# Optimization experiments

Measured on AMD Instinct MI355X. Metric: run time of the kernel, lower is better.

## Reference

```python
import jax, jax.numpy as jnp
import numpy as np

B, T, P, W = 32, 4096, 512, 1024  # batch, time, param_size, width


def setup_inputs() -> dict:
    key = jax.random.key(0)
    ks = jax.random.split(key, 9)
    lim = 1.0 / np.sqrt(W).astype(np.float32)
    lim = float(lim)
    u = lambda k, shape, l: jax.random.uniform(k, shape, minval=-l, maxval=l, dtype=jnp.float32)
    a = jax.random.normal(ks[0], (B, T, P), dtype=jnp.float32)
    h0 = u(ks[1], (W,), lim)
    weight_ih = u(ks[2], (3 * W, P), lim)
    weight_hh = u(ks[3], (3 * W, W), lim)
    bias = u(ks[4], (3 * W,), lim)
    bias_n = u(ks[5], (W,), lim)
    lim_o = float(1.0 / np.sqrt(W))
    w_out = u(ks[6], (P, W), lim_o)
    b_out = u(ks[7], (P,), lim_o)
    return {"a": a, "h0": h0, "weight_ih": weight_ih, "weight_hh": weight_hh,
            "bias": bias, "bias_n": bias_n, "w_out": w_out, "b_out": b_out}


def _encode(a, h0, weight_ih, weight_hh, bias, bias_n, w_out, b_out):
    # Precompute input gates for all steps (big GEMM, hoisted out of the scan).
    # ig: [B, T, 3W]
    ig = jnp.einsum('btp,gp->btg', a, weight_ih) + bias

    def step(h, ig_t):
        # h: [B, W], ig_t: [B, 3W]
        hg = h @ weight_hh.T                       # [B, 3W]
        ig_r, ig_z, ig_n = jnp.split(ig_t, 3, axis=-1)
        hg_r, hg_z, hg_n = jnp.split(hg, 3, axis=-1)
        r = jax.nn.sigmoid(ig_r + hg_r)
        z = jax.nn.sigmoid(ig_z + hg_z)
        n = jnp.tanh(ig_n + r * (hg_n + bias_n))
        h_new = n + z * (h - n)                    # equinox GRUCell update
        return h_new, h_new

    h_init = jnp.broadcast_to(h0, (a.shape[0], h0.shape[0]))
    # scan over time (reverse), batched inside: xs [T, B, 3W]
    _, hs = jax.lax.scan(step, h_init, jnp.swapaxes(ig, 0, 1), reverse=True)
    hs = jnp.swapaxes(hs, 0, 1)                    # [B, T, W]
    return hs @ w_out.T + b_out                    # [B, T, P]


def reference(a, h0, weight_ih, weight_hh, bias, bias_n, w_out, b_out):
    return _encode(a, h0, weight_ih, weight_hh, bias, bias_n, w_out, b_out)
```

## Files before the change

### kernel.cpp

```cpp
#include <hip/hip_runtime.h>
#include <cstddef>

#define TT 4096
#define PP 512
#define WW 1024

using u32 = unsigned;
using u64 = unsigned long long;
using u16 = unsigned short;

typedef short short8 __attribute__((ext_vector_type(8)));
typedef float f32x4 __attribute__((ext_vector_type(4)));

__device__ __forceinline__ u32 bfround(float f) {
    u32 u = __float_as_uint(f);
    return (u + 0x7fffu + ((u >> 16) & 1u)) >> 16;
}
__device__ __forceinline__ float bf2f(u32 q) { return __uint_as_float(q << 16); }
__device__ __forceinline__ float bflo(u32 q) { return __uint_as_float(q << 16); }
__device__ __forceinline__ float bfhi(u32 q) { return __uint_as_float(q & 0xffff0000u); }

#define LDA64(p)    __hip_atomic_load((p),  __ATOMIC_RELAXED, __HIP_MEMORY_SCOPE_AGENT)
#define STA64(p, v) __hip_atomic_store((p), (v), __ATOMIC_RELAXED, __HIP_MEMORY_SCOPE_AGENT)
#define LDA32(p)    __hip_atomic_load((p),  __ATOMIC_RELAXED, __HIP_MEMORY_SCOPE_AGENT)
#define STA32(p, v) __hip_atomic_store((p), (v), __ATOMIC_RELAXED, __HIP_MEMORY_SCOPE_AGENT)
#define STA16(p, v) __hip_atomic_store((p), (v), __ATOMIC_RELAXED, __HIP_MEMORY_SCOPE_AGENT)

__global__ __launch_bounds__(256) void a2bf(const float* __restrict__ a, u16* __restrict__ abf) {
    const size_t i = ((size_t)blockIdx.x * 256 + threadIdx.x) * 8;
    float4 lo = *(const float4*)&a[i];
    float4 hi = *(const float4*)&a[i + 4];
    uint4 w;
    w.x = bfround(lo.x) | (bfround(lo.y) << 16);
    w.y = bfround(lo.z) | (bfround(lo.w) << 16);
    w.z = bfround(hi.x) | (bfround(hi.y) << 16);
    w.w = bfround(hi.z) | (bfround(hi.w) << 16);
    *(uint4*)&abf[i] = w;
}

__global__ __launch_bounds__(768, 1) void ig_prepass8(
    const u16* __restrict__ abf, const float* __restrict__ Wih,
    const float* __restrict__ bias, char* __restrict__ igbase)
{
    const int gp  = blockIdx.x;
    const int t0  = blockIdx.y * 64;
    const int tid = threadIdx.x;
    const int lane = tid & 63;
    const int wid  = tid >> 6;

    short8 af[2][16];
    float  bi[2][4];
    int    gWGv[2], slotv[2];
    #pragma unroll
    for (int rt2 = 0; rt2 < 2; ++rt2) {
        const int rowb = gp * 384 + rt2 * 192 + wid * 16;
        const float* wr = &Wih[(size_t)(rowb + (lane & 15)) * PP + (lane >> 4) * 8];
        #pragma unroll
        for (int s = 0; s < 16; ++s) {
            float t8[8];
            *(float4*)&t8[0] = *(const float4*)&wr[s * 32];
            *(float4*)&t8[4] = *(const float4*)&wr[s * 32 + 4];
            #pragma unroll
            for (int j = 0; j < 8; ++j) af[rt2][s][j] = (short)bfround(t8[j]);
        }
        const int grow0 = rowb + (lane >> 4) * 4;
        #pragma unroll
        for (int r = 0; r < 4; ++r) bi[rt2][r] = bias[grow0 + r];
        const int gate = grow0 >> 10, w = grow0 & 1023;
        gWGv[rt2] = w >> 4;
        slotv[rt2] = gate * 16 + (w & 15);
    }
    const int bcol = lane & 15;

    for (int ct = 0; ct < 128; ++ct) {
        const int t = t0 + (ct >> 1);
        const int b = (ct & 1) * 16 + bcol;
        const u16* ap = &abf[((size_t)b * TT + t) * PP + (lane >> 4) * 8];
        f32x4 d0 = {0.f, 0.f, 0.f, 0.f}, d1 = {0.f, 0.f, 0.f, 0.f};
        #pragma unroll 4
        for (int s = 0; s < 16; ++s) {
            short8 bf = *(const short8*)&ap[s * 32];
            d0 = __builtin_amdgcn_mfma_f32_16x16x32_bf16(af[0][s], bf, d0, 0, 0, 0);
            d1 = __builtin_amdgcn_mfma_f32_16x16x32_bf16(af[1][s], bf, d1, 0, 0, 0);
        }
        u32 l0 = bfround(d0[0] + bi[0][0]) | (bfround(d0[1] + bi[0][1]) << 16);
        u32 h0_ = bfround(d0[2] + bi[0][2]) | (bfround(d0[3] + bi[0][3]) << 16);
        u32 l1 = bfround(d1[0] + bi[1][0]) | (bfround(d1[1] + bi[1][1]) << 16);
        u32 h1_ = bfround(d1[2] + bi[1][2]) | (bfround(d1[3] + bi[1][3]) << 16);
        *(u64*)(igbase + (((size_t)t * 64 + gWGv[0]) * 1536 + (size_t)b * 48 + slotv[0]) * 2) = (u64)l0 | ((u64)h0_ << 32);
        *(u64*)(igbase + (((size_t)t * 64 + gWGv[1]) * 1536 + (size_t)b * 48 + slotv[1]) * 2) = (u64)l1 | ((u64)h1_ << 32);
    }
}

__global__ __launch_bounds__(768, 1) void ig_prepass16(
    const float* __restrict__ a, const float* __restrict__ Wih,
    const float* __restrict__ bias, char* __restrict__ igbase)
{
    const int gp   = blockIdx.x;
    const int t0   = blockIdx.y * 64;
    const int tid  = threadIdx.x;
    const int lane = tid & 63;
    const int wid  = tid >> 6;
    const int growb = gp * 192 + wid * 16;

    short8 afrag[16];
    float  biasv[4];
    {
        const float* wr = &Wih[(size_t)(growb + (lane & 15)) * PP + (lane >> 4) * 8];
        #pragma unroll
        for (int s = 0; s < 16; ++s) {
            float t8[8];
            *(float4*)&t8[0] = *(const float4*)&wr[s * 32];
            *(float4*)&t8[4] = *(const float4*)&wr[s * 32 + 4];
            #pragma unroll
            for (int j = 0; j < 8; ++j) afrag[s][j] = (short)bfround(t8[j]);
        }
        #pragma unroll
        for (int r = 0; r < 4; ++r) biasv[r] = bias[growb + (lane >> 4) * 4 + r];
    }
    const int grow0 = growb + (lane >> 4) * 4;
    const int gate  = grow0 >> 10;
    const int w     = grow0 & 1023;
    const int gWG   = w >> 4;
    const int slot  = gate * 16 + (w & 15);
    const int bcol  = lane & 15;

    for (int ct = 0; ct < 128; ++ct) {
        const int t = t0 + (ct >> 1);
        const int b = (ct & 1) * 16 + bcol;
        const float* ap = &a[((size_t)b * TT + t) * PP + (lane >> 4) * 8];
        f32x4 d = {0.f, 0.f, 0.f, 0.f};
        #pragma unroll 4
        for (int s = 0; s < 16; ++s) {
            float4 lo = *(const float4*)&ap[s * 32];
            float4 hi = *(const float4*)&ap[s * 32 + 4];
            short8 bfv;
            bfv[0] = (short)((__float_as_uint(lo.x) + 0x8000u) >> 16);
            bfv[1] = (short)((__float_as_uint(lo.y) + 0x8000u) >> 16);
            bfv[2] = (short)((__float_as_uint(lo.z) + 0x8000u) >> 16);
            bfv[3] = (short)((__float_as_uint(lo.w) + 0x8000u) >> 16);
            bfv[4] = (short)((__float_as_uint(hi.x) + 0x8000u) >> 16);
            bfv[5] = (short)((__float_as_uint(hi.y) + 0x8000u) >> 16);
            bfv[6] = (short)((__float_as_uint(hi.z) + 0x8000u) >> 16);
            bfv[7] = (short)((__float_as_uint(hi.w) + 0x8000u) >> 16);
            d = __builtin_amdgcn_mfma_f32_16x16x32_bf16(afrag[s], bfv, d, 0, 0, 0);
        }
        u32 lo32 = bfround(d[0] + biasv[0]) | (bfround(d[1] + biasv[1]) << 16);
        u32 hi32 = bfround(d[2] + biasv[2]) | (bfround(d[3] + biasv[3]) << 16);
        *(u64*)(igbase + (((size_t)t * 64 + gWG) * 1536 + (size_t)b * 48 + slot) * 2) =
            (u64)lo32 | ((u64)hi32 << 32);
    }
}

__global__ __launch_bounds__(768, 1) void gru_scan4(
    const float* __restrict__ h0v, const float* __restrict__ Whh,
    const float* __restrict__ bias_n, const float* __restrict__ Wout,
    const float* __restrict__ bout, const char* __restrict__ igbase,
    float* __restrict__ out, u64* __restrict__ bufA, u64* __restrict__ bufB,
    u32* __restrict__ flags)
{
    __shared__ float sPreH[4][48][2][17];
    __shared__ float sOutP[4][16][18];
    __shared__ __align__(8) u64 sIgRaw[384];

    const int g    = blockIdx.x;
    const int tid  = threadIdx.x;
    const int lane = tid & 63;
    const int wid  = tid >> 6;
    const int p0   = (g >> 1) * 16;
    const int pb0  = (g & 1) * 16;

    short8 frag[24];
    if (wid < 8) {
        const int kq = wid & 3;
        #pragma unroll
        for (int gate = 0; gate < 3; ++gate)
            #pragma unroll
            for (int s = 0; s < 8; ++s) {
                const float* wr = &Whh[(size_t)(gate * WW + g * 16 + (lane & 15)) * WW
                                       + (kq * 8 + s) * 32 + (lane >> 4) * 8];
                float t8[8];
                *(float4*)&t8[0] = *(const float4*)&wr[0];
                *(float4*)&t8[4] = *(const float4*)&wr[4];
                short8 v;
                #pragma unroll
                for (int j = 0; j < 8; ++j) v[j] = (short)bfround(t8[j]);
                frag[gate * 8 + s] = v;
            }
    } else {
        const int kq3 = wid - 8;
        #pragma unroll
        for (int s = 0; s < 8; ++s) {
            const float* wr = &Wout[(size_t)(p0 + (lane & 15)) * WW
                                    + (kq3 * 8 + s) * 32 + (lane >> 4) * 8];
            float t8[8];
            *(float4*)&t8[0] = *(const float4*)&wr[0];
            *(float4*)&t8[4] = *(const float4*)&wr[4];
            short8 v;
            #pragma unroll
            for (int j = 0; j < 8; ++j) v[j] = (short)bfround(t8[j]);
            frag[s] = v;
        }
    }

    float h_own = 0.f, bnv = 0.f;
    int gwl = 0, gb = 0; u32 hidx16 = 0;
    if (tid >= 256) {
        const int idx = tid - 256;
        gwl = idx & 15; gb = idx >> 4;
        h_own = h0v[g * 16 + gwl];
        bnv   = bias_n[g * 16 + gwl];
        const int w_abs = g * 16 + gwl;
        const int ip = (w_abs >> 3) * 64 + 2 * gb + ((w_abs >> 2) & 1);
        hidx16 = 4 * ip + (w_abs & 3);
        STA16(&((u16*)bufA)[hidx16], (u16)bfround(h_own));
    }
    const float boutp = (tid < 256) ? bout[p0 + (tid & 15)] : 0.f;

    const int fo_hh = (lane >> 4) * 32 + ((wid >> 2) & 1) * 16 + (lane & 15);
    const int fo_p3 = (lane >> 4) * 32 + pb0 + (lane & 15);

    u64* hcur = bufA;
    u64* hnxt = bufB;
    u32 kk = 1;

    for (int t = TT - 1; t >= 0; --t) {
        if (wid >= 4) asm volatile("s_waitcnt vmcnt(0)" ::: "memory");
        __syncthreads();
        if (tid == 0) STA32(&flags[g * 16], kk);

        u64 igr = 0;
        if (tid < 384) igr = *(const u64*)(igbase + ((size_t)t * 64 + g) * 3072 + tid * 8);

        for (;;) {
            u32 v = LDA32(&flags[lane * 16]);
            if (__all((int)(v - kk) >= 0)) break;
            __builtin_amdgcn_s_sleep(1);
        }
        asm volatile("" ::: "memory");

        if (wid < 8) {
            const int kq = wid & 3;
            f32x4 c0 = {0.f,0.f,0.f,0.f}, c1 = {0.f,0.f,0.f,0.f}, c2 = {0.f,0.f,0.f,0.f};
            #pragma unroll
            for (int s = 0; s < 8; ++s) {
                const int ss = kq * 8 + s;
                const u64 q0 = LDA64(&hcur[2 * (ss * 128 + fo_hh)]);
                const u64 q1 = LDA64(&hcur[2 * (ss * 128 + fo_hh) + 1]);
                union { u64 q[2]; short8 v; } uu; uu.q[0] = q0; uu.q[1] = q1;
                c0 = __builtin_amdgcn_mfma_f32_16x16x32_bf16(frag[s],      uu.v, c0, 0, 0, 0);
                c1 = __builtin_amdgcn_mfma_f32_16x16x32_bf16(frag[8 + s],  uu.v, c1, 0, 0, 0);
                c2 = __builtin_amdgcn_mfma_f32_16x16x32_bf16(frag[16 + s], uu.v, c2, 0, 0, 0);
            }
            const int bt = wid >> 2, r0 = (lane >> 4) * 4, col = lane & 15;
            #pragma unroll
            for (int r = 0; r < 4; ++r) {
                sPreH[kq][r0 + r][bt][col]      = c0[r];
                sPreH[kq][16 + r0 + r][bt][col] = c1[r];
                sPreH[kq][32 + r0 + r][bt][col] = c2[r];
            }
        } else {
            const int kq3 = wid - 8;
            f32x4 d = {0.f, 0.f, 0.f, 0.f};
            #pragma unroll
            for (int s = 0; s < 8; ++s) {
                const int ss = kq3 * 8 + s;
                const u64 q0 = LDA64(&hcur[2 * (ss * 128 + fo_p3)]);
                const u64 q1 = LDA64(&hcur[2 * (ss * 128 + fo_p3) + 1]);
                union { u64 q[2]; short8 v; } uu; uu.q[0] = q0; uu.q[1] = q1;
                d = __builtin_amdgcn_mfma_f32_16x16x32_bf16(frag[s], uu.v, d, 0, 0, 0);
            }
            const int r0 = (lane >> 4) * 4, col = lane & 15;
            #pragma unroll
            for (int r = 0; r < 4; ++r) sOutP[kq3][r0 + r][col] = d[r];
        }
        if (tid < 384) sIgRaw[tid] = igr;
        __syncthreads();

        if (tid >= 256) {
            const u16* sIgU = (const u16*)sIgRaw;
            const float ig_r = bf2f(sIgU[gb * 48 + gwl]);
            const float ig_z = bf2f(sIgU[gb * 48 + 16 + gwl]);
            const float ig_n = bf2f(sIgU[gb * 48 + 32 + gwl]);
            const int bh = gb >> 4, bc = gb & 15;
            const float hg_r = sPreH[0][gwl][bh][bc] + sPreH[1][gwl][bh][bc]
                             + sPreH[2][gwl][bh][bc] + sPreH[3][gwl][bh][bc];
            const float hg_z = sPreH[0][16 + gwl][bh][bc] + sPreH[1][16 + gwl][bh][bc]
                             + sPreH[2][16 + gwl][bh][bc] + sPreH[3][16 + gwl][bh][bc];
            const float hg_n = sPreH[0][32 + gwl][bh][bc] + sPreH[1][32 + gwl][bh][bc]
                             + sPreH[2][32 + gwl][bh][bc] + sPreH[3][32 + gwl][bh][bc];
            const float rr = __builtin_amdgcn_rcpf(1.f + __expf(-(ig_r + hg_r)));
            const float zz = __builtin_amdgcn_rcpf(1.f + __expf(-(ig_z + hg_z)));
            const float xn = ig_n + rr * (hg_n + bnv);
            const float nn = 2.f * __builtin_amdgcn_rcpf(1.f + __expf(-2.f * xn)) - 1.f;
            h_own = nn + zz * (h_own - nn);
            STA16(&((u16*)hnxt)[hidx16], (u16)bfround(h_own));
        } else if (t < TT - 1) {
            const int p = tid & 15, b = tid >> 4;
            const float s_ = boutp + sOutP[0][p][b] + sOutP[1][p][b]
                                   + sOutP[2][p][b] + sOutP[3][p][b];
            out[((size_t)(pb0 + b) * TT + (t + 1)) * PP + p0 + p] = s_;
        }

        u64* tmp = hcur; hcur = hnxt; hnxt = tmp;
        ++kk;
    }

    if (wid >= 4) asm volatile("s_waitcnt vmcnt(0)" ::: "memory");
    __syncthreads();
    if (tid == 0) STA32(&flags[g * 16], kk);
    if (wid >= 8) {
        for (;;) {
            u32 v = LDA32(&flags[lane * 16]);
            if (__all((int)(v - kk) >= 0)) break;
            __builtin_amdgcn_s_sleep(1);
        }
        asm volatile("" ::: "memory");
        const int kq3 = wid - 8;
        f32x4 d = {0.f, 0.f, 0.f, 0.f};
        #pragma unroll
        for (int s = 0; s < 8; ++s) {
            const int ss = kq3 * 8 + s;
            const u64 q0 = LDA64(&hcur[2 * (ss * 128 + fo_p3)]);
            const u64 q1 = LDA64(&hcur[2 * (ss * 128 + fo_p3) + 1]);
            union { u64 q[2]; short8 v; } uu; uu.q[0] = q0; uu.q[1] = q1;
            d = __builtin_amdgcn_mfma_f32_16x16x32_bf16(frag[s], uu.v, d, 0, 0, 0);
        }
        const int r0 = (lane >> 4) * 4, col = lane & 15;
        #pragma unroll
        for (int r = 0; r < 4; ++r) sOutP[kq3][r0 + r][col] = d[r];
    }
    __syncthreads();
    if (tid < 256) {
        const int p = tid & 15, b = tid >> 4;
        const float s_ = boutp + sOutP[0][p][b] + sOutP[1][p][b]
                               + sOutP[2][p][b] + sOutP[3][p][b];
        out[((size_t)(pb0 + b) * TT) * PP + p0 + p] = s_;
    }
}

__device__ __forceinline__ void grid_barrier32(u32* leaf, u32* root, u32 rtarget, int g) {
    asm volatile("s_waitcnt vmcnt(0)" ::: "memory");
    __syncthreads();
    if (threadIdx.x == 0) {
        u32 old = __hip_atomic_fetch_add(&leaf[(g & 7) * 16], 1u,
                                         __ATOMIC_RELAXED, __HIP_MEMORY_SCOPE_AGENT);
        if ((old & 31u) == 31u)
            __hip_atomic_fetch_add(root, 1u, __ATOMIC_RELAXED, __HIP_MEMORY_SCOPE_AGENT);
        while (__hip_atomic_load(root, __ATOMIC_RELAXED, __HIP_MEMORY_SCOPE_AGENT) < rtarget)
            __builtin_amdgcn_s_sleep(2);
    }
    __syncthreads();
}

__global__ __launch_bounds__(768, 1) void gru_scan_fb(
    const float* __restrict__ a, const float* __restrict__ h0,
    const float* __restrict__ Wih, const float* __restrict__ Whh,
    const float* __restrict__ bias, const float* __restrict__ bias_n,
    const float* __restrict__ Wout, const float* __restrict__ bout,
    float* __restrict__ out, u64* __restrict__ hbufA, u64* __restrict__ hbufB,
    u32* __restrict__ leaf, u32* __restrict__ root)
{
    __shared__ float sWhh[12][WW];
    __shared__ __align__(16) u64 sh[8192];
    __shared__ float sPreH[2][12][32];
    __shared__ float sIg[2][2][12][32];
    __shared__ float sOutPart[12][64];

    const int g   = blockIdx.x;
    const int tid = threadIdx.x;
// ... 142 lines not shown
        r5 = LDH(5); r6 = LDH(6); r7 = LDH(7); r8 = LDH(8); r9 = LDH(9);
        if (tid < 512) r10 = LDH(10);
        #undef LDH
        sh[tid] = r0;          sh[tid + 768] = r1;   sh[tid + 1536] = r2;
        sh[tid + 2304] = r3;   sh[tid + 3072] = r4;  sh[tid + 3840] = r5;
        sh[tid + 4608] = r6;   sh[tid + 5376] = r7;  sh[tid + 6144] = r8;
        sh[tid + 6912] = r9;
        if (tid < 512) sh[tid + 7680] = r10;
        __syncthreads();
        p3partials();
        __syncthreads();
        if (tid < 64) {
            float s_ = boutv;
            #pragma unroll
            for (int cc = 0; cc < 12; ++cc) s_ += sOutPart[cc][o];
            out[((size_t)p3b * TT) * PP + p3p] = s_;
        }
    }
}

extern "C" void kernel_launch(void* const* d_in, const int* in_sizes, int n_in,
                              void* d_out, int out_size, void* d_ws, size_t ws_size,
                              hipStream_t stream) {
    const float* a      = (const float*)d_in[0];
    const float* h0     = (const float*)d_in[1];
    const float* Wih    = (const float*)d_in[2];
    const float* Whh    = (const float*)d_in[3];
    const float* bias   = (const float*)d_in[4];
    const float* bias_n = (const float*)d_in[5];
    const float* Wout   = (const float*)d_in[6];
    const float* bout   = (const float*)d_in[7];
    float* out = (float*)d_out;

    const size_t IG_BYTES  = (size_t)TT * 64 * 3072;
    const size_t ABF_BYTES = (size_t)32 * TT * PP * 2;
    const size_t NEED_FULL = IG_BYTES + ABF_BYTES + 2 * 65536 + 4096;
    const size_t NEED_MID  = IG_BYTES + 2 * 65536 + 4096;

    if (ws_size >= NEED_FULL) {
        char* igbase = (char*)d_ws;
        u16*  abf    = (u16*)((char*)d_ws + IG_BYTES);
        u64*  bufA   = (u64*)((char*)d_ws + IG_BYTES + ABF_BYTES);
        u64*  bufB   = bufA + 8192;
        u32*  flags  = (u32*)((char*)d_ws + IG_BYTES + ABF_BYTES + 2 * 65536);
        hipMemsetAsync(flags, 0, 4096, stream);
        hipLaunchKernelGGL(a2bf, dim3(32768), dim3(256), 0, stream, a, abf);
        hipLaunchKernelGGL(ig_prepass8, dim3(8, 64), dim3(768), 0, stream,
                           abf, Wih, bias, igbase);
        void* args[] = {(void*)&h0, (void*)&Whh, (void*)&bias_n, (void*)&Wout,
                        (void*)&bout, (void*)&igbase, (void*)&out,
                        (void*)&bufA, (void*)&bufB, (void*)&flags};
        hipLaunchCooperativeKernel((void*)gru_scan4, dim3(64), dim3(768),
                                   args, 0, stream);
    } else if (ws_size >= NEED_MID) {
        char* igbase = (char*)d_ws;
        u64*  bufA   = (u64*)((char*)d_ws + IG_BYTES);
        u64*  bufB   = bufA + 8192;
        u32*  flags  = (u32*)((char*)d_ws + IG_BYTES + 2 * 65536);
        hipMemsetAsync(flags, 0, 4096, stream);
        hipLaunchKernelGGL(ig_prepass16, dim3(16, 64), dim3(768), 0, stream,
                           a, Wih, bias, igbase);
        void* args[] = {(void*)&h0, (void*)&Whh, (void*)&bias_n, (void*)&Wout,
                        (void*)&bout, (void*)&igbase, (void*)&out,
                        (void*)&bufA, (void*)&bufB, (void*)&flags};
        hipLaunchCooperativeKernel((void*)gru_scan4, dim3(64), dim3(768),
                                   args, 0, stream);
    } else {
        u64* hA   = (u64*)d_ws;
        u64* hB   = hA + 8192;
        u32* leaf = (u32*)((char*)d_ws + 2 * 65536);
        u32* root = leaf + 8 * 16;
        hipMemsetAsync(leaf, 0, 1024, stream);
        void* args[] = {(void*)&a, (void*)&h0, (void*)&Wih, (void*)&Whh,
                        (void*)&bias, (void*)&bias_n, (void*)&Wout, (void*)&bout,
                        (void*)&out, (void*)&hA, (void*)&hB, (void*)&leaf, (void*)&root};
        hipLaunchCooperativeKernel((void*)gru_scan_fb, dim3(256), dim3(768),
                                   args, 0, stream);
    }
}
```

Before: 20.30 ms.

## Fuse input-gate GEMM producer blocks with GRU scan in one cooperative kernel

Replaces the separate a-to-bf16 conversion, input-gate prepass and scan kernels with a single cooperative kernel of 256 blocks. Blocks 0-63 run the recurrence while the other blocks compute the input-gate GEMM per 64-step chunk in reverse time order and signal readiness through counters. The old global flag barrier is replaced by tagged h values that consumers poll until the step tag matches, and the output projection is folded into the same MFMA loop. This overlaps the large prepass with the serial scan and removes launches and the bf16 staging buffer, at the cost of spin-wait polling, more register pressure, and producers that can fall behind the scan.

```diff
diff --git a/kernel.cpp b/kernel.cpp
--- a/kernel.cpp
+++ b/kernel.cpp
@@ -24,155 +24,43 @@
 #define STA64(p, v) __hip_atomic_store((p), (v), __ATOMIC_RELAXED, __HIP_MEMORY_SCOPE_AGENT)
 #define LDA32(p)    __hip_atomic_load((p),  __ATOMIC_RELAXED, __HIP_MEMORY_SCOPE_AGENT)
 #define STA32(p, v) __hip_atomic_store((p), (v), __ATOMIC_RELAXED, __HIP_MEMORY_SCOPE_AGENT)
-#define STA16(p, v) __hip_atomic_store((p), (v), __ATOMIC_RELAXED, __HIP_MEMORY_SCOPE_AGENT)
-
-__global__ __launch_bounds__(256) void a2bf(const float* __restrict__ a, u16* __restrict__ abf) {
-    const size_t i = ((size_t)blockIdx.x * 256 + threadIdx.x) * 8;
-    float4 lo = *(const float4*)&a[i];
-    float4 hi = *(const float4*)&a[i + 4];
-    uint4 w;
-    w.x = bfround(lo.x) | (bfround(lo.y) << 16);
-    w.y = bfround(lo.z) | (bfround(lo.w) << 16);
-    w.z = bfround(hi.x) | (bfround(hi.y) << 16);
-    w.w = bfround(hi.z) | (bfround(hi.w) << 16);
-    *(uint4*)&abf[i] = w;
-}
-
-__global__ __launch_bounds__(768, 1) void ig_prepass8(
-    const u16* __restrict__ abf, const float* __restrict__ Wih,
-    const float* __restrict__ bias, char* __restrict__ igbase)
-{
-    const int gp  = blockIdx.x;
-    const int t0  = blockIdx.y * 64;
-    const int tid = threadIdx.x;
-    const int lane = tid & 63;
-    const int wid  = tid >> 6;
-
-    short8 af[2][16];
-    float  bi[2][4];
-    int    gWGv[2], slotv[2];
-    #pragma unroll
-    for (int rt2 = 0; rt2 < 2; ++rt2) {
-        const int rowb = gp * 384 + rt2 * 192 + wid * 16;
-        const float* wr = &Wih[(size_t)(rowb + (lane & 15)) * PP + (lane >> 4) * 8];
-        #pragma unroll
-        for (int s = 0; s < 16; ++s) {
-            float t8[8];
-            *(float4*)&t8[0] = *(const float4*)&wr[s * 32];
-            *(float4*)&t8[4] = *(const float4*)&wr[s * 32 + 4];
-            #pragma unroll
-            for (int j = 0; j < 8; ++j) af[rt2][s][j] = (short)bfround(t8[j]);
-        }
-        const int grow0 = rowb + (lane >> 4) * 4;
-        #pragma unroll
-        for (int r = 0; r < 4; ++r) bi[rt2][r] = bias[grow0 + r];
-        const int gate = grow0 >> 10, w = grow0 & 1023;
-        gWGv[rt2] = w >> 4;
-        slotv[rt2] = gate * 16 + (w & 15);
-    }
-    const int bcol = lane & 15;
-
-    for (int ct = 0; ct < 128; ++ct) {
-        const int t = t0 + (ct >> 1);
-        const int b = (ct & 1) * 16 + bcol;
-        const u16* ap = &abf[((size_t)b * TT + t) * PP + (lane >> 4) * 8];
-        f32x4 d0 = {0.f, 0.f, 0.f, 0.f}, d1 = {0.f, 0.f, 0.f, 0.f};
-        #pragma unroll 4
-        for (int s = 0; s < 16; ++s) {
-            short8 bf = *(const short8*)&ap[s * 32];
-            d0 = __builtin_amdgcn_mfma_f32_16x16x32_bf16(af[0][s], bf, d0, 0, 0, 0);
-            d1 = __builtin_amdgcn_mfma_f32_16x16x32_bf16(af[1][s], bf, d1, 0, 0, 0);
-        }
-        u32 l0 = bfround(d0[0] + bi[0][0]) | (bfround(d0[1] + bi[0][1]) << 16);
-        u32 h0_ = bfround(d0[2] + bi[0][2]) | (bfround(d0[3] + bi[0][3]) << 16);
-        u32 l1 = bfround(d1[0] + bi[1][0]) | (bfround(d1[1] + bi[1][1]) << 16);
-        u32 h1_ = bfround(d1[2] + bi[1][2]) | (bfround(d1[3] + bi[1][3]) << 16);
-        *(u64*)(igbase + (((size_t)t * 64 + gWGv[0]) * 1536 + (size_t)b * 48 + slotv[0]) * 2) = (u64)l0 | ((u64)h0_ << 32);
-        *(u64*)(igbase + (((size_t)t * 64 + gWGv[1]) * 1536 + (size_t)b * 48 + slotv[1]) * 2) = (u64)l1 | ((u64)h1_ << 32);
-    }
-}
-
-__global__ __launch_bounds__(768, 1) void ig_prepass16(
-    const float* __restrict__ a, const float* __restrict__ Wih,
-    const float* __restrict__ bias, char* __restrict__ igbase)
-{
-    const int gp   = blockIdx.x;
-    const int t0   = blockIdx.y * 64;
-    const int tid  = threadIdx.x;
-    const int lane = tid & 63;
-    const int wid  = tid >> 6;
-    const int growb = gp * 192 + wid * 16;
-
-    short8 afrag[16];
-    float  biasv[4];
-    {
-        const float* wr = &Wih[(size_t)(growb + (lane & 15)) * PP + (lane >> 4) * 8];
-        #pragma unroll
-        for (int s = 0; s < 16; ++s) {
-            float t8[8];
-            *(float4*)&t8[0] = *(const float4*)&wr[s * 32];
-            *(float4*)&t8[4] = *(const float4*)&wr[s * 32 + 4];
-            #pragma unroll
-            for (int j = 0; j < 8; ++j) afrag[s][j] = (short)bfround(t8[j]);
-        }
-        #pragma unroll
-        for (int r = 0; r < 4; ++r) biasv[r] = bias[growb + (lane >> 4) * 4 + r];
-    }
-    const int grow0 = growb + (lane >> 4) * 4;
-    const int gate  = grow0 >> 10;
-    const int w     = grow0 & 1023;
-    const int gWG   = w >> 4;
-    const int slot  = gate * 16 + (w & 15);
-    const int bcol  = lane & 15;
-
-    for (int ct = 0; ct < 128; ++ct) {
-        const int t = t0 + (ct >> 1);
-        const int b = (ct & 1) * 16 + bcol;
-        const float* ap = &a[((size_t)b * TT + t) * PP + (lane >> 4) * 8];
-        f32x4 d = {0.f, 0.f, 0.f, 0.f};
-        #pragma unroll 4
-        for (int s = 0; s < 16; ++s) {
-            float4 lo = *(const float4*)&ap[s * 32];
-            float4 hi = *(const float4*)&ap[s * 32 + 4];
-            short8 bfv;
-            bfv[0] = (short)((__float_as_uint(lo.x) + 0x8000u) >> 16);
-            bfv[1] = (short)((__float_as_uint(lo.y) + 0x8000u) >> 16);
-            bfv[2] = (short)((__float_as_uint(lo.z) + 0x8000u) >> 16);
-            bfv[3] = (short)((__float_as_uint(lo.w) + 0x8000u) >> 16);
-            bfv[4] = (short)((__float_as_uint(hi.x) + 0x8000u) >> 16);
-            bfv[5] = (short)((__float_as_uint(hi.y) + 0x8000u) >> 16);
-            bfv[6] = (short)((__float_as_uint(hi.z) + 0x8000u) >> 16);
-            bfv[7] = (short)((__float_as_uint(hi.w) + 0x8000u) >> 16);
-            d = __builtin_amdgcn_mfma_f32_16x16x32_bf16(afrag[s], bfv, d, 0, 0, 0);
-        }
-        u32 lo32 = bfround(d[0] + biasv[0]) | (bfround(d[1] + biasv[1]) << 16);
-        u32 hi32 = bfround(d[2] + biasv[2]) | (bfround(d[3] + biasv[3]) << 16);
-        *(u64*)(igbase + (((size_t)t * 64 + gWG) * 1536 + (size_t)b * 48 + slot) * 2) =
-            (u64)lo32 | ((u64)hi32 << 32);
-    }
-}
-
-__global__ __launch_bounds__(768, 1) void gru_scan4(
-    const float* __restrict__ h0v, const float* __restrict__ Whh,
-    const float* __restrict__ bias_n, const float* __restrict__ Wout,
-    const float* __restrict__ bout, const char* __restrict__ igbase,
-    float* __restrict__ out, u64* __restrict__ bufA, u64* __restrict__ bufB,
-    u32* __restrict__ flags)
+
+#define TAGM 0x00001FFF00001FFFull
+
+__global__ __launch_bounds__(512, 2) void gru_fused(
+    const float* __restrict__ a,
+    const float* __restrict__ h0v,
+    const float* __restrict__ Wih,
+    const float* __restrict__ Whh,
+    const float* __restrict__ bias,
+    const float* __restrict__ bias_n,
+    const float* __restrict__ Wout,
+    const float* __restrict__ bout,
+    char* __restrict__ igbase,
+    float* __restrict__ out,
+    u64* __restrict__ bufA, u64* __restrict__ bufB,
+    u32* __restrict__ igready)
 {
     __shared__ float sPreH[4][48][2][17];
     __shared__ float sOutP[4][16][18];
     __shared__ __align__(8) u64 sIgRaw[384];
-
-    const int g    = blockIdx.x;
+    __shared__ __align__(16) u16 aLds[16][520];
+
+    const int bid  = blockIdx.x;
     const int tid  = threadIdx.x;
     const int lane = tid & 63;
     const int wid  = tid >> 6;
-    const int p0   = (g >> 1) * 16;
-    const int pb0  = (g & 1) * 16;
-
-    short8 frag[24];
-    if (wid < 8) {
-        const int kq = wid & 3;
+
+    if (bid < 64) {
+        const int g   = bid;
+        const int kq  = wid & 3;
+        const int bt  = wid >> 2;
+        const int p0  = (g >> 1) * 16;
+        const int pb0 = (g & 1) * 16;
+        const bool isP3 = (bt == (g & 1));
+        const int colb  = bt * 16 + (lane & 15);
+
+        short8 fragR[8], fragZ[8], fragN[8], fragP[8];
         #pragma unroll
         for (int gate = 0; gate < 3; ++gate)
             #pragma unroll
@@ -185,157 +73,268 @@
                 short8 v;
                 #pragma unroll
                 for (int j = 0; j < 8; ++j) v[j] = (short)bfround(t8[j]);
-                frag[gate * 8 + s] = v;
-            }
-    } else {
-        const int kq3 = wid - 8;
-        #pragma unroll
-        for (int s = 0; s < 8; ++s) {
-            const float* wr = &Wout[(size_t)(p0 + (lane & 15)) * WW
-                                    + (kq3 * 8 + s) * 32 + (lane >> 4) * 8];
-            float t8[8];
-            *(float4*)&t8[0] = *(const float4*)&wr[0];
-            *(float4*)&t8[4] = *(const float4*)&wr[4];
-            short8 v;
-            #pragma unroll
-            for (int j = 0; j < 8; ++j) v[j] = (short)bfround(t8[j]);
-            frag[s] = v;
-        }
-    }
-
-    float h_own = 0.f, bnv = 0.f;
-    int gwl = 0, gb = 0; u32 hidx16 = 0;
-    if (tid >= 256) {
-        const int idx = tid - 256;
-        gwl = idx & 15; gb = idx >> 4;
-        h_own = h0v[g * 16 + gwl];
-        bnv   = bias_n[g * 16 + gwl];
-        const int w_abs = g * 16 + gwl;
-        const int ip = (w_abs >> 3) * 64 + 2 * gb + ((w_abs >> 2) & 1);
-        hidx16 = 4 * ip + (w_abs & 3);
-        STA16(&((u16*)bufA)[hidx16], (u16)bfround(h_own));
-    }
-    const float boutp = (tid < 256) ? bout[p0 + (tid & 15)] : 0.f;
-
-    const int fo_hh = (lane >> 4) * 32 + ((wid >> 2) & 1) * 16 + (lane & 15);
-    const int fo_p3 = (lane >> 4) * 32 + pb0 + (lane & 15);
-
-    u64* hcur = bufA;
-    u64* hnxt = bufB;
-    u32 kk = 1;
-
-    for (int t = TT - 1; t >= 0; --t) {
-        if (wid >= 4) asm volatile("s_waitcnt vmcnt(0)" ::: "memory");
+                if (gate == 0) fragR[s] = v; else if (gate == 1) fragZ[s] = v; else fragN[s] = v;
+            }
+        if (isP3) {
+            #pragma unroll
+            for (int s = 0; s < 8; ++s) {
+                const float* wr = &Wout[(size_t)(p0 + (lane & 15)) * WW
+                                        + (kq * 8 + s) * 32 + (lane >> 4) * 8];
+                float t8[8];
+                *(float4*)&t8[0] = *(const float4*)&wr[0];
+                *(float4*)&t8[4] = *(const float4*)&wr[4];
+                short8 v;
+                #pragma unroll
+                for (int j = 0; j < 8; ++j) v[j] = (short)bfround(t8[j]);
+                fragP[s] = v;
+            }
+        }
+
+        const int gwl = tid & 15, gb = tid >> 4;
+        float h_own = h0v[g * 16 + gwl];
+        const float bnv = bias_n[g * 16 + gwl];
+        const int pubW = (g * 2 + (gwl >> 3)) * 256 + gb * 8 + (gwl & 7);
+        const float boutp = (tid < 256) ? bout[p0 + (tid & 15)] : 0.f;
+
+        STA32(&((u32*)bufA)[pubW], (bfround(h_own) << 16) | 4097u);
+
+        u64* cur = bufA;
+        u64* nxt = bufB;
+
+        for (int t = TT - 1; t >= 0; --t) {
+            if ((t & 63) == 63 && tid < 384) {
+                while (LDA32(&igready[(t >> 6) * 16]) < 8u)
+                    __builtin_amdgcn_s_sleep(8);
+            }
+            u64 igr = 0;
+            if (tid < 384) igr = *(const u64*)(igbase + ((size_t)t * 64 + g) * 3072 + tid * 8);
+
+            const u32 tg = (u32)(t + 2);
+            const u64 want2 = (u64)tg | ((u64)tg << 32);
+            f32x4 cR = {0.f,0.f,0.f,0.f}, cZ = {0.f,0.f,0.f,0.f};
+            f32x4 cN = {0.f,0.f,0.f,0.f}, cP = {0.f,0.f,0.f,0.f};
+            #pragma unroll
+            for (int grp = 0; grp < 2; ++grp) {
+                u64 q[16];
+                #pragma unroll
+                for (int s4 = 0; s4 < 4; ++s4) {
+                    const int ss = kq * 8 + grp * 4 + s4;
+                    const int ub = (ss * 4 + (lane >> 4)) * 128 + colb * 4;
+                    #pragma unroll
+                    for (int j = 0; j < 4; ++j) q[s4 * 4 + j] = LDA64(&cur[ub + j]);
+                }
+                bool ok;
+                do {
+                    ok = true;
+                    #pragma unroll
+                    for (int s4 = 0; s4 < 4; ++s4) {
+                        const int ss = kq * 8 + grp * 4 + s4;
+                        const int ub = (ss * 4 + (lane >> 4)) * 128 + colb * 4;
+                        #pragma unroll
+                        for (int j = 0; j < 4; ++j)
+                            if (((q[s4 * 4 + j] ^ want2) & TAGM) != 0ull) {
+                                q[s4 * 4 + j] = LDA64(&cur[ub + j]); ok = false;
+                            }
+                    }
+                } while (!__all(ok));
+                #pragma unroll
+                for (int s4 = 0; s4 < 4; ++s4) {
+                    const int s = grp * 4 + s4;
+                    const u64 a0 = q[s4*4+0], a1 = q[s4*4+1], a2 = q[s4*4+2], a3 = q[s4*4+3];
+                    short8 bv;
+                    bv[0] = (short)((u32)a0 >> 16); bv[1] = (short)(a0 >> 48);
+                    bv[2] = (short)((u32)a1 >> 16); bv[3] = (short)(a1 >> 48);
+                    bv[4] = (short)((u32)a2 >> 16); bv[5] = (short)(a2 >> 48);
+                    bv[6] = (short)((u32)a3 >> 16); bv[7] = (short)(a3 >> 48);
+                    cR = __builtin_amdgcn_mfma_f32_16x16x32_bf16(fragR[s], bv, cR, 0, 0, 0);
+                    cZ = __builtin_amdgcn_mfma_f32_16x16x32_bf16(fragZ[s], bv, cZ, 0, 0, 0);
+                    cN = __builtin_amdgcn_mfma_f32_16x16x32_bf16(fragN[s], bv, cN, 0, 0, 0);
+                    if (isP3 && t < TT - 1)
+                        cP = __builtin_amdgcn_mfma_f32_16x16x32_bf16(fragP[s], bv, cP, 0, 0, 0);
+                }
+            }
+            {
+                const int r0 = (lane >> 4) * 4, col = lane & 15;
+                #pragma unroll
+                for (int r = 0; r < 4; ++r) {
+                    sPreH[kq][r0 + r][bt][col]      = cR[r];
+                    sPreH[kq][16 + r0 + r][bt][col] = cZ[r];
+                    sPreH[kq][32 + r0 + r][bt][col] = cN[r];
+                }
+                if (isP3 && t < TT - 1) {
+                    #pragma unroll
+                    for (int r = 0; r < 4; ++r) sOutP[kq][r0 + r][col] = cP[r];
+                }
+            }
+            if (tid < 384) sIgRaw[tid] = igr;
+            __syncthreads();
+
+            {
+                const u16* sIgU = (const u16*)sIgRaw;
+                const float ig_r = bf2f(sIgU[gb * 48 + gwl]);
+                const float ig_z = bf2f(sIgU[gb * 48 + 16 + gwl]);
+                const float ig_n = bf2f(sIgU[gb * 48 + 32 + gwl]);
+                const int bh = gb >> 4, bc = gb & 15;
+                const float hg_r = sPreH[0][gwl][bh][bc] + sPreH[1][gwl][bh][bc]
+                                 + sPreH[2][gwl][bh][bc] + sPreH[3][gwl][bh][bc];
+                const float hg_z = sPreH[0][16 + gwl][bh][bc] + sPreH[1][16 + gwl][bh][bc]
+                                 + sPreH[2][16 + gwl][bh][bc] + sPreH[3][16 + gwl][bh][bc];
+                const float hg_n = sPreH[0][32 + gwl][bh][bc] + sPreH[1][32 + gwl][bh][bc]
+                                 + sPreH[2][32 + gwl][bh][bc] + sPreH[3][32 + gwl][bh][bc];
+                const float rr = __builtin_amdgcn_rcpf(1.f + __expf(-(ig_r + hg_r)));
+                const float zz = __builtin_amdgcn_rcpf(1.f + __expf(-(ig_z + hg_z)));
+                const float xn = ig_n + rr * (hg_n + bnv);
+                const float nn = 2.f * __builtin_amdgcn_rcpf(1.f + __expf(-2.f * xn)) - 1.f;
+                h_own = nn + zz * (h_own - nn);
+                STA32(&((u32*)nxt)[pubW], (bfround(h_own) << 16) | (u32)(t + 1));
+            }
+            if (t < TT - 1 && tid < 256) {
+                const int p = tid & 15, b = tid >> 4;
+                const float s_ = boutp + sOutP[0][p][b] + sOutP[1][p][b]
+                                       + sOutP[2][p][b] + sOutP[3][p][b];
+                out[((size_t)(pb0 + b) * TT + (t + 1)) * PP + p0 + p] = s_;
+            }
+            __syncthreads();
+
+            u64* tmp = cur; cur = nxt; nxt = tmp;
+        }
+
+        if (isP3) {
+            const u64 want2 = 1ull | (1ull << 32);
+            f32x4 cP = {0.f, 0.f, 0.f, 0.f};
+            #pragma unroll
+            for (int grp = 0; grp < 2; ++grp) {
+                u64 q[16];
+                #pragma unroll
+                for (int s4 = 0; s4 < 4; ++s4) {
+                    const int ss = kq * 8 + grp * 4 + s4;
+                    const int ub = (ss * 4 + (lane >> 4)) * 128 + colb * 4;
+                    #pragma unroll
+                    for (int j = 0; j < 4; ++j) q[s4 * 4 + j] = LDA64(&cur[ub + j]);
+                }
+                bool ok;
+                do {
+                    ok = true;
+                    #pragma unroll
+                    for (int s4 = 0; s4 < 4; ++s4) {
+                        const int ss = kq * 8 + grp * 4 + s4;
+                        const int ub = (ss * 4 + (lane >> 4)) * 128 + colb * 4;
+                        #pragma unroll
+                        for (int j = 0; j < 4; ++j)
+                            if (((q[s4 * 4 + j] ^ want2) & TAGM) != 0ull) {
+                                q[s4 * 4 + j] = LDA64(&cur[ub + j]); ok = false;
+                            }
+                    }
+                } while (!__all(ok));
+                #pragma unroll
+                for (int s4 = 0; s4 < 4; ++s4) {
+                    const int s = grp * 4 + s4;
+                    const u64 a0 = q[s4*4+0], a1 = q[s4*4+1], a2 = q[s4*4+2], a3 = q[s4*4+3];
+                    short8 bv;
+                    bv[0] = (short)((u32)a0 >> 16); bv[1] = (short)(a0 >> 48);
+                    bv[2] = (short)((u32)a1 >> 16); bv[3] = (short)(a1 >> 48);
+                    bv[4] = (short)((u32)a2 >> 16); bv[5] = (short)(a2 >> 48);
+                    bv[6] = (short)((u32)a3 >> 16); bv[7] = (short)(a3 >> 48);
+                    cP = __builtin_amdgcn_mfma_f32_16x16x32_bf16(fragP[s], bv, cP, 0, 0, 0);
+                }
+            }
+            const int r0 = (lane >> 4) * 4, col = lane & 15;
+            #pragma unroll
+            for (int r = 0; r < 4; ++r) sOutP[kq][r0 + r][col] = cP[r];
+        }
         __syncthreads();
-        if (tid == 0) STA32(&flags[g * 16], kk);
-
-        u64 igr = 0;
-        if (tid < 384) igr = *(const u64*)(igbase + ((size_t)t * 64 + g) * 3072 + tid * 8);
-
-        for (;;) {
-            u32 v = LDA32(&flags[lane * 16]);
-            if (__all((int)(v - kk) >= 0)) break;
-            __builtin_amdgcn_s_sleep(1);
-        }
-        asm volatile("" ::: "memory");
-
-        if (wid < 8) {
-            const int kq = wid & 3;
-            f32x4 c0 = {0.f,0.f,0.f,0.f}, c1 = {0.f,0.f,0.f,0.f}, c2 = {0.f,0.f,0.f,0.f};
-            #pragma unroll
-            for (int s = 0; s < 8; ++s) {
-                const int ss = kq * 8 + s;
-                const u64 q0 = LDA64(&hcur[2 * (ss * 128 + fo_hh)]);
-                const u64 q1 = LDA64(&hcur[2 * (ss * 128 + fo_hh) + 1]);
-                union { u64 q[2]; short8 v; } uu; uu.q[0] = q0; uu.q[1] = q1;
-                c0 = __builtin_amdgcn_mfma_f32_16x16x32_bf16(frag[s],      uu.v, c0, 0, 0, 0);
-                c1 = __builtin_amdgcn_mfma_f32_16x16x32_bf16(frag[8 + s],  uu.v, c1, 0, 0, 0);
-                c2 = __builtin_amdgcn_mfma_f32_16x16x32_bf16(frag[16 + s], uu.v, c2, 0, 0, 0);
-            }
-            const int bt = wid >> 2, r0 = (lane >> 4) * 4, col = lane & 15;
-            #pragma unroll
-            for (int r = 0; r < 4; ++r) {
-                sPreH[kq][r0 + r][bt][col]      = c0[r];
-                sPreH[kq][16 + r0 + r][bt][col] = c1[r];
-                sPreH[kq][32 + r0 + r][bt][col] = c2[r];
-            }
-        } else {
-            const int kq3 = wid - 8;
-            f32x4 d = {0.f, 0.f, 0.f, 0.f};
-            #pragma unroll
-            for (int s = 0; s < 8; ++s) {
-                const int ss = kq3 * 8 + s;
-                const u64 q0 = LDA64(&hcur[2 * (ss * 128 + fo_p3)]);
-                const u64 q1 = LDA64(&hcur[2 * (ss * 128 + fo_p3) + 1]);
-                union { u64 q[2]; short8 v; } uu; uu.q[0] = q0; uu.q[1] = q1;
-                d = __builtin_amdgcn_mfma_f32_16x16x32_bf16(frag[s], uu.v, d, 0, 0, 0);
-            }
-            const int r0 = (lane >> 4) * 4, col = lane & 15;
-            #pragma unroll
-            for (int r = 0; r < 4; ++r) sOutP[kq3][r0 + r][col] = d[r];
-        }
-        if (tid < 384) sIgRaw[tid] = igr;
-        __syncthreads();
-
-        if (tid >= 256) {
-            const u16* sIgU = (const u16*)sIgRaw;
-            const float ig_r = bf2f(sIgU[gb * 48 + gwl]);
-            const float ig_z = bf2f(sIgU[gb * 48 + 16 + gwl]);
-            const float ig_n = bf2f(sIgU[gb * 48 + 32 + gwl]);
-            const int bh = gb >> 4, bc = gb & 15;
-            const float hg_r = sPreH[0][gwl][bh][bc] + sPreH[1][gwl][bh][bc]
-                             + sPreH[2][gwl][bh][bc] + sPreH[3][gwl][bh][bc];
-            const float hg_z = sPreH[0][16 + gwl][bh][bc] + sPreH[1][16 + gwl][bh][bc]
-                             + sPreH[2][16 + gwl][bh][bc] + sPreH[3][16 + gwl][bh][bc];
-            const float hg_n = sPreH[0][32 + gwl][bh][bc] + sPreH[1][32 + gwl][bh][bc]
-                             + sPreH[2][32 + gwl][bh][bc] + sPreH[3][32 + gwl][bh][bc];
-            const float rr = __builtin_amdgcn_rcpf(1.f + __expf(-(ig_r + hg_r)));
-            const float zz = __builtin_amdgcn_rcpf(1.f + __expf(-(ig_z + hg_z)));
-            const float xn = ig_n + rr * (hg_n + bnv);
-            const float nn = 2.f * __builtin_amdgcn_rcpf(1.f + __expf(-2.f * xn)) - 1.f;
-            h_own = nn + zz * (h_own - nn);
-            STA16(&((u16*)hnxt)[hidx16], (u16)bfround(h_own));
-        } else if (t < TT - 1) {
+        if (tid < 256) {
             const int p = tid & 15, b = tid >> 4;
             const float s_ = boutp + sOutP[0][p][b] + sOutP[1][p][b]
                                    + sOutP[2][p][b] + sOutP[3][p][b];
-            out[((size_t)(pb0 + b) * TT + (t + 1)) * PP + p0 + p] = s_;
-        }
-
-        u64* tmp = hcur; hcur = hnxt; hnxt = tmp;
-        ++kk;
-    }
-
-    if (wid >= 4) asm volatile("s_waitcnt vmcnt(0)" ::: "memory");
-    __syncthreads();
-    if (tid == 0) STA32(&flags[g * 16], kk);
-    if (wid >= 8) {
-        for (;;) {
-            u32 v = LDA32(&flags[lane * 16]);
-            if (__all((int)(v - kk) >= 0)) break;
-            __builtin_amdgcn_s_sleep(1);
-        }
-        asm volatile("" ::: "memory");
-        const int kq3 = wid - 8;
-        f32x4 d = {0.f, 0.f, 0.f, 0.f};
+            out[((size_t)(pb0 + b) * TT) * PP + p0 + p] = s_;
+        }
+    } else {
+        const int pid = bid - 64;
+        const int gp  = pid & 7;
+
+        short8 af[3][16];
+        float  bi[3][4];
+        int    gWGv[3], slotv[3];
         #pragma unroll
-        for (int s = 0; s < 8; ++s) {
-            const int ss = kq3 * 8 + s;
-            const u64 q0 = LDA64(&hcur[2 * (ss * 128 + fo_p3)]);
-            const u64 q1 = LDA64(&hcur[2 * (ss * 128 + fo_p3) + 1]);
-            union { u64 q[2]; short8 v; } uu; uu.q[0] = q0; uu.q[1] = q1;
-            d = __builtin_amdgcn_mfma_f32_16x16x32_bf16(frag[s], uu.v, d, 0, 0, 0);
-        }
-        const int r0 = (lane >> 4) * 4, col = lane & 15;
-        #pragma unroll
-        for (int r = 0; r < 4; ++r) sOutP[kq3][r0 + r][col] = d[r];
-    }
-    __syncthreads();
-    if (tid < 256) {
-        const int p = tid & 15, b = tid >> 4;
-        const float s_ = boutp + sOutP[0][p][b] + sOutP[1][p][b]
-                               + sOutP[2][p][b] + sOutP[3][p][b];
-        out[((size_t)(pb0 + b) * TT) * PP + p0 + p] = s_;
+        for (int r3 = 0; r3 < 3; ++r3) {
+            const int rowb = gp * 384 + (wid * 3 + r3) * 16;
+            const float* wr = &Wih[(size_t)(rowb + (lane & 15)) * PP + (lane >> 4) * 8];
+            #pragma unroll
+            for (int s = 0; s < 16; ++s) {
+                float t8[8];
+                *(float4*)&t8[0] = *(const float4*)&wr[s * 32];
+                *(float4*)&t8[4] = *(const float4*)&wr[s * 32 + 4];
+                #pragma unroll
+                for (int j = 0; j < 8; ++j) af[r3][s][j] = (short)bfround(t8[j]);
+            }
+            const int grow0 = rowb + (lane >> 4) * 4;
+            #pragma unroll
+            for (int r = 0; r < 4; ++r) bi[r3][r] = bias[grow0 + r];
+            const int gate = grow0 >> 10, w = grow0 & 1023;
+            gWGv[r3]  = w >> 4;
+            slotv[r3] = gate * 16 + (w & 15);
+        }
+        const int b_loc = tid >> 5;
+        const int pc    = tid & 31;
+        const int bcol  = lane & 15;
+
+        for (int vb = pid; vb < 512; vb += 192) {
+            const int tb = 63 - (vb >> 3);
+            for (int ct = 0; ct < 128; ++ct) {
+                const int t  = tb * 64 + (ct >> 1);
+                const int bh = ct & 1;
+                {
+                    const int b = bh * 16 + b_loc;
+                    const float* ap = &a[((size_t)b * TT + t) * PP + pc * 16];
+                    float4 f0 = *(const float4*)&ap[0];
+                    float4 f1 = *(const float4*)&ap[4];
+                    float4 f2 = *(const float4*)&ap[8];
+                    float4 f3 = *(const float4*)&ap[12];
+                    uint4 w0, w1;
+                    w0.x = bfround(f0.x) | (bfround(f0.y) << 16);
+                    w0.y = bfround(f0.z) | (bfround(f0.w) << 16);
+                    w0.z = bfround(f1.x) | (bfround(f1.y) << 16);
+                    w0.w = bfround(f1.z) | (bfround(f1.w) << 16);
+                    w1.x = bfround(f2.x) | (bfround(f2.y) << 16);
+                    w1.y = bfround(f2.z) | (bfround(f2.w) << 16);
+                    w1.z = bfround(f3.x) | (bfround(f3.y) << 16);
+                    w1.w = bfround(f3.z) | (bfround(f3.w) << 16);
+                    *(uint4*)&aLds[b_loc][pc * 16]     = w0;
+                    *(uint4*)&aLds[b_loc][pc * 16 + 8] = w1;
+                }
+                __syncthreads();
+                f32x4 d0 = {0.f,0.f,0.f,0.f}, d1 = {0.f,0.f,0.f,0.f}, d2 = {0.f,0.f,0.f,0.f};
+                #pragma unroll 4
+                for (int s = 0; s < 16; ++s) {
+                    short8 bfrag = *(const short8*)&aLds[lane & 15][s * 32 + (lane >> 4) * 8];
+                    d0 = __builtin_amdgcn_mfma_f32_16x16x32_bf16(af[0][s], bfrag, d0, 0, 0, 0);
+                    d1 = __builtin_amdgcn_mfma_f32_16x16x32_bf16(af[1][s], bfrag, d1, 0, 0, 0);
+                    d2 = __builtin_amdgcn_mfma_f32_16x16x32_bf16(af[2][s], bfrag, d2, 0, 0, 0);
+                }
+                {
+                    const int b = bh * 16 + bcol;
+                    u32 l0 = bfround(d0[0] + bi[0][0]) | (bfround(d0[1] + bi[0][1]) << 16);
+                    u32 h0_ = bfround(d0[2] + bi[0][2]) | (bfround(d0[3] + bi[0][3]) << 16);
+                    u32 l1 = bfround(d1[0] + bi[1][0]) | (bfround(d1[1] + bi[1][1]) << 16);
+                    u32 h1_ = bfround(d1[2] + bi[1][2]) | (bfround(d1[3] + bi[1][3]) << 16);
+                    u32 l2 = bfround(d2[0] + bi[2][0]) | (bfround(d2[1] + bi[2][1]) << 16);
+                    u32 h2_ = bfround(d2[2] + bi[2][2]) | (bfround(d2[3] + bi[2][3]) << 16);
+                    STA64((u64*)(igbase + (((size_t)t * 64 + gWGv[0]) * 1536 + (size_t)b * 48 + slotv[0]) * 2),
+                          (u64)l0 | ((u64)h0_ << 32));
+                    STA64((u64*)(igbase + (((size_t)t * 64 + gWGv[1]) * 1536 + (size_t)b * 48 + slotv[1]) * 2),
+                          (u64)l1 | ((u64)h1_ << 32));
+                    STA64((u64*)(igbase + (((size_t)t * 64 + gWGv[2]) * 1536 + (size_t)b * 48 + slotv[2]) * 2),
+                          (u64)l2 | ((u64)h2_ << 32));
+                }
+                __syncthreads();
+            }
+            asm volatile("s_waitcnt vmcnt(0)" ::: "memory");
+            __syncthreads();
+            if (tid == 0)
+                __hip_atomic_fetch_add(&igready[tb * 16], 1u,
+                                       __ATOMIC_RELAXED, __HIP_MEMORY_SCOPE_AGENT);
+        }
     }
 }
 
@@ -545,37 +544,20 @@
     float* out = (float*)d_out;
 
     const size_t IG_BYTES  = (size_t)TT * 64 * 3072;
-    const size_t ABF_BYTES = (size_t)32 * TT * PP * 2;
-    const size_t NEED_FULL = IG_BYTES + ABF_BYTES + 2 * 65536 + 4096;
-    const size_t NEED_MID  = IG_BYTES + 2 * 65536 + 4096;
-
-    if (ws_size >= NEED_FULL) {
-        char* igbase = (char*)d_ws;
-        u16*  abf    = (u16*)((char*)d_ws + IG_BYTES);
-        u64*  bufA   = (u64*)((char*)d_ws + IG_BYTES + ABF_BYTES);
-        u64*  bufB   = bufA + 8192;
-        u32*  flags  = (u32*)((char*)d_ws + IG_BYTES + ABF_BYTES + 2 * 65536);
-        hipMemsetAsync(flags, 0, 4096, stream);
-        hipLaunchKernelGGL(a2bf, dim3(32768), dim3(256), 0, stream, a, abf);
-        hipLaunchKernelGGL(ig_prepass8, dim3(8, 64), dim3(768), 0, stream,
-                           abf, Wih, bias, igbase);
-        void* args[] = {(void*)&h0, (void*)&Whh, (void*)&bias_n, (void*)&Wout,
-                        (void*)&bout, (void*)&igbase, (void*)&out,
-                        (void*)&bufA, (void*)&bufB, (void*)&flags};
-        hipLaunchCooperativeKernel((void*)gru_scan4, dim3(64), dim3(768),
-                                   args, 0, stream);
-    } else if (ws_size >= NEED_MID) {
-        char* igbase = (char*)d_ws;
-        u64*  bufA   = (u64*)((char*)d_ws + IG_BYTES);
-        u64*  bufB   = bufA + 8192;
-        u32*  flags  = (u32*)((char*)d_ws + IG_BYTES + 2 * 65536);
-        hipMemsetAsync(flags, 0, 4096, stream);
-        hipLaunchKernelGGL(ig_prepass16, dim3(16, 64), dim3(768), 0, stream,
-                           a, Wih, bias, igbase);
-        void* args[] = {(void*)&h0, (void*)&Whh, (void*)&bias_n, (void*)&Wout,
-                        (void*)&bout, (void*)&igbase, (void*)&out,
-                        (void*)&bufA, (void*)&bufB, (void*)&flags};
-        hipLaunchCooperativeKernel((void*)gru_scan4, dim3(64), dim3(768),
+    const size_t BUF_BYTES = 131072;
+    const size_t NEED = IG_BYTES + 2 * BUF_BYTES + 4096;
+
+    if (ws_size >= NEED) {
+        char* igbase  = (char*)d_ws;
+        u64*  bufA    = (u64*)((char*)d_ws + IG_BYTES);
+        u64*  bufB    = (u64*)((char*)d_ws + IG_BYTES + BUF_BYTES);
+        u32*  igready = (u32*)((char*)d_ws + IG_BYTES + 2 * BUF_BYTES);
+        hipMemsetAsync(bufA, 0, 2 * BUF_BYTES + 4096, stream);
+        void* args[] = {(void*)&a, (void*)&h0, (void*)&Wih, (void*)&Whh,
+                        (void*)&bias, (void*)&bias_n, (void*)&Wout, (void*)&bout,
+                        (void*)&igbase, (void*)&out,
+                        (void*)&bufA, (void*)&bufB, (void*)&igready};
+        hipLaunchCooperativeKernel((void*)gru_fused, dim3(256), dim3(512),
                                    args, 0, stream);
     } else {
         u64* hA   = (u64*)d_ws;
```

Measured after the change: 26.41 ms. 1.3x slower.

## Transpose bf16 input into MFMA-fragment layout and defer output stores a step

Applied to the files above, without the earlier changes.

The bf16 conversion kernel now also transposes the input into a per-timestep layout grouped by k-chunk, so each MFMA B-fragment load in the input-gate prepass reads contiguous 16-byte blocks instead of strided rows. In the scan kernel, the output projection store for the first 256 threads moves to the top of the next iteration and writes step t+2, taking it off the gate-computation path, with a tail store after the loop. This adds a shared-memory transpose pass and depends on sOutP not being overwritten before it is read.

```diff
diff --git a/kernel.cpp b/kernel.cpp
--- a/kernel.cpp
+++ b/kernel.cpp
@@ -26,20 +26,39 @@
 #define STA32(p, v) __hip_atomic_store((p), (v), __ATOMIC_RELAXED, __HIP_MEMORY_SCOPE_AGENT)
 #define STA16(p, v) __hip_atomic_store((p), (v), __ATOMIC_RELAXED, __HIP_MEMORY_SCOPE_AGENT)
 
-__global__ __launch_bounds__(256) void a2bf(const float* __restrict__ a, u16* __restrict__ abf) {
-    const size_t i = ((size_t)blockIdx.x * 256 + threadIdx.x) * 8;
-    float4 lo = *(const float4*)&a[i];
-    float4 hi = *(const float4*)&a[i + 4];
-    uint4 w;
-    w.x = bfround(lo.x) | (bfround(lo.y) << 16);
-    w.y = bfround(lo.z) | (bfround(lo.w) << 16);
-    w.z = bfround(hi.x) | (bfround(hi.y) << 16);
-    w.w = bfround(hi.z) | (bfround(hi.w) << 16);
-    *(uint4*)&abf[i] = w;
-}
-
-__global__ __launch_bounds__(768, 1) void ig_prepass8(
-    const u16* __restrict__ abf, const float* __restrict__ Wih,
+__global__ __launch_bounds__(256, 2) void a2bf_t(const float* __restrict__ a,
+                                                 u16* __restrict__ abf2) {
+    __shared__ u16 sh[32][528];
+
+    const int t   = blockIdx.x;
+    const int tid = threadIdx.x;
+
+    {
+        const int b = tid >> 3, seg = tid & 7;
+        const float* ap = &a[((size_t)b * TT + t) * PP + seg * 64];
+        #pragma unroll
+        for (int j = 0; j < 16; ++j) {
+            float4 v = *(const float4*)&ap[j * 4];
+            uint2 w;
+            w.x = bfround(v.x) | (bfround(v.y) << 16);
+            w.y = bfround(v.z) | (bfround(v.w) << 16);
+            *(uint2*)&sh[b][seg * 64 + j * 4] = w;
+        }
+    }
+    __syncthreads();
+    {
+        const int d = tid >> 2, bq = tid & 3;
+        #pragma unroll
+        for (int bb = 0; bb < 8; ++bb) {
+            const int b = bq * 8 + bb;
+            uint4 v = *(const uint4*)&sh[b][d * 8];
+            *(uint4*)&abf2[(((size_t)t * 64 + d) * 32 + b) * 8] = v;
+        }
+    }
+}
+
+__global__ __launch_bounds__(768, 1) void ig_prepass9(
+    const u16* __restrict__ abf2, const float* __restrict__ Wih,
     const float* __restrict__ bias, char* __restrict__ igbase)
 {
     const int gp  = blockIdx.x;
@@ -47,6 +66,8 @@
     const int tid = threadIdx.x;
     const int lane = tid & 63;
     const int wid  = tid >> 6;
+    const int lq   = lane >> 4;
+    const int bcol = lane & 15;
 
     short8 af[2][16];
     float  bi[2][4];
@@ -54,7 +75,7 @@
     #pragma unroll
     for (int rt2 = 0; rt2 < 2; ++rt2) {
         const int rowb = gp * 384 + rt2 * 192 + wid * 16;
-        const float* wr = &Wih[(size_t)(rowb + (lane & 15)) * PP + (lane >> 4) * 8];
+        const float* wr = &Wih[(size_t)(rowb + bcol) * PP + lq * 8];
         #pragma unroll
         for (int s = 0; s < 16; ++s) {
             float t8[8];
@@ -63,23 +84,22 @@
             #pragma unroll
             for (int j = 0; j < 8; ++j) af[rt2][s][j] = (short)bfround(t8[j]);
         }
-        const int grow0 = rowb + (lane >> 4) * 4;
+        const int grow0 = rowb + lq * 4;
         #pragma unroll
         for (int r = 0; r < 4; ++r) bi[rt2][r] = bias[grow0 + r];
         const int gate = grow0 >> 10, w = grow0 & 1023;
-        gWGv[rt2] = w >> 4;
+        gWGv[rt2]  = w >> 4;
         slotv[rt2] = gate * 16 + (w & 15);
     }
-    const int bcol = lane & 15;
 
     for (int ct = 0; ct < 128; ++ct) {
         const int t = t0 + (ct >> 1);
         const int b = (ct & 1) * 16 + bcol;
-        const u16* ap = &abf[((size_t)b * TT + t) * PP + (lane >> 4) * 8];
+        const u16* bp = &abf2[(((size_t)t * 64 + lq) * 32 + b) * 8];
         f32x4 d0 = {0.f, 0.f, 0.f, 0.f}, d1 = {0.f, 0.f, 0.f, 0.f};
         #pragma unroll 4
         for (int s = 0; s < 16; ++s) {
-            short8 bf = *(const short8*)&ap[s * 32];
+            short8 bf = *(const short8*)&bp[(size_t)s * 4 * 256];
             d0 = __builtin_amdgcn_mfma_f32_16x16x32_bf16(af[0][s], bf, d0, 0, 0, 0);
             d1 = __builtin_amdgcn_mfma_f32_16x16x32_bf16(af[1][s], bf, d1, 0, 0, 0);
         }
@@ -225,6 +245,13 @@
     u32 kk = 1;
 
     for (int t = TT - 1; t >= 0; --t) {
+        if (t < TT - 2 && tid < 256) {
+            const int p = tid & 15, b = tid >> 4;
+            float s_ = boutp;
+            #pragma unroll
+            for (int cc = 0; cc < 4; ++cc) s_ += sOutP[cc][p][b];
+            out[((size_t)(pb0 + b) * TT + (t + 2)) * PP + p0 + p] = s_;
+        }
         if (wid >= 4) asm volatile("s_waitcnt vmcnt(0)" ::: "memory");
         __syncthreads();
         if (tid == 0) STA32(&flags[g * 16], kk);
@@ -295,17 +322,19 @@
             const float nn = 2.f * __builtin_amdgcn_rcpf(1.f + __expf(-2.f * xn)) - 1.f;
             h_own = nn + zz * (h_own - nn);
             STA16(&((u16*)hnxt)[hidx16], (u16)bfround(h_own));
-        } else if (t < TT - 1) {
-            const int p = tid & 15, b = tid >> 4;
-            const float s_ = boutp + sOutP[0][p][b] + sOutP[1][p][b]
-                                   + sOutP[2][p][b] + sOutP[3][p][b];
-            out[((size_t)(pb0 + b) * TT + (t + 1)) * PP + p0 + p] = s_;
         }
 
         u64* tmp = hcur; hcur = hnxt; hnxt = tmp;
         ++kk;
     }
 
+    if (tid < 256) {
+        const int p = tid & 15, b = tid >> 4;
+        float s_ = boutp;
+        #pragma unroll
+        for (int cc = 0; cc < 4; ++cc) s_ += sOutP[cc][p][b];
+        out[((size_t)(pb0 + b) * TT + 1) * PP + p0 + p] = s_;
+    }
     if (wid >= 4) asm volatile("s_waitcnt vmcnt(0)" ::: "memory");
     __syncthreads();
     if (tid == 0) STA32(&flags[g * 16], kk);
@@ -544,21 +573,21 @@
     const float* bout   = (const float*)d_in[7];
     float* out = (float*)d_out;
 
-    const size_t IG_BYTES  = (size_t)TT * 64 * 3072;
-    const size_t ABF_BYTES = (size_t)32 * TT * PP * 2;
-    const size_t NEED_FULL = IG_BYTES + ABF_BYTES + 2 * 65536 + 4096;
-    const size_t NEED_MID  = IG_BYTES + 2 * 65536 + 4096;
+    const size_t IG_BYTES   = (size_t)TT * 64 * 3072;
+    const size_t ABF2_BYTES = (size_t)TT * 64 * 32 * 8 * 2;
+    const size_t NEED_FULL  = IG_BYTES + ABF2_BYTES + 2 * 65536 + 4096;
+    const size_t NEED_MID   = IG_BYTES + 2 * 65536 + 4096;
 
     if (ws_size >= NEED_FULL) {
         char* igbase = (char*)d_ws;
-        u16*  abf    = (u16*)((char*)d_ws + IG_BYTES);
-        u64*  bufA   = (u64*)((char*)d_ws + IG_BYTES + ABF_BYTES);
+        u16*  abf2   = (u16*)((char*)d_ws + IG_BYTES);
+        u64*  bufA   = (u64*)((char*)d_ws + IG_BYTES + ABF2_BYTES);
         u64*  bufB   = bufA + 8192;
-        u32*  flags  = (u32*)((char*)d_ws + IG_BYTES + ABF_BYTES + 2 * 65536);
+        u32*  flags  = (u32*)((char*)d_ws + IG_BYTES + ABF2_BYTES + 2 * 65536);
         hipMemsetAsync(flags, 0, 4096, stream);
-        hipLaunchKernelGGL(a2bf, dim3(32768), dim3(256), 0, stream, a, abf);
-        hipLaunchKernelGGL(ig_prepass8, dim3(8, 64), dim3(768), 0, stream,
-                           abf, Wih, bias, igbase);
+        hipLaunchKernelGGL(a2bf_t, dim3(TT), dim3(256), 0, stream, a, abf2);
+        hipLaunchKernelGGL(ig_prepass9, dim3(8, 64), dim3(768), 0, stream,
+                           abf2, Wih, bias, igbase);
         void* args[] = {(void*)&h0, (void*)&Whh, (void*)&bias_n, (void*)&Wout,
                         (void*)&bout, (void*)&igbase, (void*)&out,
                         (void*)&bufA, (void*)&bufB, (void*)&flags};
```

After: 19.97 ms. About the same (-1.7%).
